# Kernel tuning notes

Hardware: AMD Instinct MI355X
Metric: run time of the kernel (lower is better)

The kernel has to match this reference:

```python
import jax, jax.numpy as jnp
import numpy as np

B, N, D_IN, D_B, K = 32, 1024, 1024, 256, 16384


def setup_inputs() -> dict:
    key = jax.random.key(0)
    ks = jax.random.split(key, 8)
    s_in = 1.0 / np.sqrt(D_IN)
    s_b = 1.0 / np.sqrt(D_B)
    return {
        "x": jax.random.normal(ks[0], (B, N, D_IN), dtype=jnp.float32),
        "W_in": jax.random.uniform(ks[1], (D_IN, D_B), jnp.float32, -s_in, s_in),
        "b_in": jax.random.uniform(ks[2], (D_B,), jnp.float32, -s_in, s_in),
        "W_out": jax.random.uniform(ks[3], (D_B, D_IN), jnp.float32, -s_b, s_b),
        "b_out": jax.random.uniform(ks[4], (D_IN,), jnp.float32, -s_b, s_b),
        "codebook": jax.random.normal(ks[5], (K, D_B), dtype=jnp.float32),
        "W_proj": jax.random.uniform(ks[6], (D_B, D_B), jnp.float32, -s_b, s_b),
        "b_proj": jax.random.uniform(ks[7], (D_B,), jnp.float32, -s_b, s_b),
    }


def reference(x, W_in, b_in, W_out, b_out, codebook, W_proj, b_proj):
    # project_in
    z = jnp.einsum('bnd,de->bne', x, W_in) + b_in            # [B,N,Db]
    # SimVQ: projected codebook
    emb = codebook @ W_proj + b_proj                          # [K,Db]
    zf = z.reshape(-1, z.shape[-1])                           # [B*N,Db]
    # squared-distance argmin (cdist pattern)
    d = (jnp.sum(zf**2, axis=1, keepdims=True)
         + jnp.sum(emb**2, axis=1)
         - 2.0 * zf @ emb.T)                                  # [B*N,K]
    q_idx = jnp.argmin(d, axis=1)                             # [B*N]
    quantized = emb[q_idx].reshape(z.shape)                   # [B,N,Db]
    # straight-through
    reg_z = z + jax.lax.stop_gradient(quantized - z)
    # project_out
    x_hat = jnp.einsum('bnd,de->bne', reg_z, W_out) + b_out   # [B,N,Dout]
    bottleneck_rep = q_idx.reshape(z.shape[0], z.shape[1])
    return x_hat, bottleneck_rep, z, emb, reg_z
```

## Files before the change

kernel.cpp:

```cpp
#include <hip/hip_runtime.h>

typedef unsigned int u32;
typedef unsigned long long u64;
typedef unsigned short u16;

#define M_ROWS 32768
#define DB 256
#define DIN 1024
#define KCODES 16384

typedef __attribute__((ext_vector_type(8))) short bf16x8;
typedef __attribute__((ext_vector_type(4))) float f32x4;
typedef __attribute__((ext_vector_type(8))) unsigned short us8;

#define GLOAD16(gp, lp) __builtin_amdgcn_global_load_lds( \
    (const __attribute__((address_space(1))) unsigned int*)(gp), \
    (__attribute__((address_space(3))) unsigned int*)(lp), 16, 0, 0)

__device__ __forceinline__ u32 ford(float f) {
    u32 u = __float_as_uint(f);
    return (u & 0x80000000u) ? ~u : (u | 0x80000000u);
}
__device__ __forceinline__ u64 shfl_xor_u64(u64 v, int m) {
    u32 lo = (u32)v, hi = (u32)(v >> 32);
    lo = (u32)__shfl_xor((int)lo, m, 64);
    hi = (u32)__shfl_xor((int)hi, m, 64);
    return ((u64)hi << 32) | lo;
}
__device__ __forceinline__ u16 f2bf_rne(float f) {
    const u32 u = __float_as_uint(f);
    return (u16)((u + 0x7FFFu + ((u >> 16) & 1u)) >> 16);
}

__global__ __launch_bounds__(256)
void sgemm_f32(const float* __restrict__ A, int lda,
               const float* __restrict__ B, int ldb,
               const float* __restrict__ bias,
               float* __restrict__ C, int ldc, int Kd)
{
    __shared__ float As[16][132];
    __shared__ float Bs[16][132];
    const int t = threadIdx.x;
    const int w = t >> 6, lane = t & 63;
    const int tx = (lane & 7) | ((w & 1) << 3);
    const int ty = ((lane >> 3) & 7) | ((w >> 1) << 3);
    const int rb = blockIdx.x << 7;
    const int cb = blockIdx.y << 7;

    const int sr  = t >> 1;
    const int sk8 = (t & 1) << 3;
    const int bkr = t >> 4;
    const int bc8 = (t & 15) << 3;

    const float* Ap = A + (size_t)(rb + sr) * lda + sk8;
    const float* Bp = B + (size_t)bkr * ldb + cb + bc8;

    float acc[8][8];
#pragma unroll
    for (int i = 0; i < 8; ++i)
#pragma unroll
        for (int j = 0; j < 8; ++j) acc[i][j] = 0.0f;

    float4 a0 = *(const float4*)Ap;
    float4 a1 = *(const float4*)(Ap + 4);
    float4 b0 = *(const float4*)Bp;
    float4 b1 = *(const float4*)(Bp + 4);

    for (int kb = 0; kb < Kd; kb += 16) {
        __syncthreads();
        As[sk8 + 0][sr] = a0.x; As[sk8 + 1][sr] = a0.y;
        As[sk8 + 2][sr] = a0.z; As[sk8 + 3][sr] = a0.w;
        As[sk8 + 4][sr] = a1.x; As[sk8 + 5][sr] = a1.y;
        As[sk8 + 6][sr] = a1.z; As[sk8 + 7][sr] = a1.w;
        *(float4*)&Bs[bkr][bc8]     = b0;
        *(float4*)&Bs[bkr][bc8 + 4] = b1;
        __syncthreads();
        if (kb + 16 < Kd) {
            a0 = *(const float4*)(Ap + kb + 16);
            a1 = *(const float4*)(Ap + kb + 20);
            b0 = *(const float4*)(Bp + (size_t)(kb + 16) * ldb);
            b1 = *(const float4*)(Bp + (size_t)(kb + 16) * ldb + 4);
        }
#pragma unroll
        for (int kk = 0; kk < 16; ++kk) {
            float a[8], b[8];
            *(float4*)&a[0] = *(const float4*)&As[kk][ty * 8];
            *(float4*)&a[4] = *(const float4*)&As[kk][ty * 8 + 4];
            *(float4*)&b[0] = *(const float4*)&Bs[kk][tx * 8];
            *(float4*)&b[4] = *(const float4*)&Bs[kk][tx * 8 + 4];
#pragma unroll
            for (int i = 0; i < 8; ++i)
#pragma unroll
                for (int j = 0; j < 8; ++j)
                    acc[i][j] += a[i] * b[j];
        }
    }

    float bb[8];
#pragma unroll
    for (int j = 0; j < 8; ++j) bb[j] = bias[cb + tx * 8 + j];

#pragma unroll
    for (int i = 0; i < 8; ++i) {
        const size_t off = (size_t)(rb + ty * 8 + i) * ldc + cb + tx * 8;
        *(float4*)&C[off]     = make_float4(acc[i][0] + bb[0], acc[i][1] + bb[1],
                                            acc[i][2] + bb[2], acc[i][3] + bb[3]);
        *(float4*)&C[off + 4] = make_float4(acc[i][4] + bb[4], acc[i][5] + bb[5],
                                            acc[i][6] + bb[6], acc[i][7] + bb[7]);
    }
}

__global__ __launch_bounds__(256)
void rowsq_kernel(const float* __restrict__ X, float* __restrict__ s2)
{
    const int t = threadIdx.x;
    const int row = (blockIdx.x << 2) + (t >> 6);
    const int lane = t & 63;
    const float4 v = *(const float4*)(X + (size_t)row * DB + (lane << 2));
    float s = v.x * v.x + v.y * v.y + v.z * v.z + v.w * v.w;
#pragma unroll
    for (int m = 32; m >= 1; m >>= 1) s += __shfl_xor(s, m, 64);
    if (lane == 0) s2[row] = s;
}

__global__ __launch_bounds__(256)
void split_pack(const float* __restrict__ X, u16* __restrict__ hi, u16* __restrict__ lo)
{
    const int tid = (blockIdx.x << 8) + threadIdx.x;
    const int row = tid >> 5;
    const int kb  = (tid & 31) << 3;
    const float4 v0 = *(const float4*)(X + ((size_t)row << 8) + kb);
    const float4 v1 = *(const float4*)(X + ((size_t)row << 8) + kb + 4);
    const float f[8] = {v0.x, v0.y, v0.z, v0.w, v1.x, v1.y, v1.z, v1.w};
    us8 hv, lv;
#pragma unroll
    for (int e = 0; e < 8; ++e) {
        const u16 h = f2bf_rne(f[e]);
        const float hf = __uint_as_float((u32)h << 16);
        hv[e] = h;
        lv[e] = f2bf_rne(f[e] - hf);
    }
    const size_t off = ((size_t)(row >> 4) * 8 + (kb >> 5)) * 512
                     + (size_t)((kb >> 3) & 3) * 128 + ((row & 15) << 3);
    *(us8*)(hi + off) = hv;
    *(us8*)(lo + off) = lv;
}

__global__ __launch_bounds__(256)
void score_mfma(const u16* __restrict__ zh, const u16* __restrict__ zl,
                const u16* __restrict__ eh, const u16* __restrict__ el,
                const float* __restrict__ e2, const float* __restrict__ z2,
                u64* __restrict__ partial)
{
    __shared__ u16 smem[4][8][512];
    const int t = threadIdx.x;
    const int w = t >> 6, lane = t & 63;
    const int wr = w >> 1, wc = w & 1;
    const int rb = blockIdx.x << 7, cb = blockIdx.y << 7;
    const u32 lane8 = (u32)lane << 3;

    const u32 zc0 = (u32)((rb >> 4) + w)     * 4096 + lane8;
    const u32 zc1 = (u32)((rb >> 4) + 4 + w) * 4096 + lane8;
    const u32 ec0 = (u32)((cb >> 4) + w)     * 4096 + lane8;
    const u32 ec1 = (u32)((cb >> 4) + 4 + w) * 4096 + lane8;

    u16* ZhL0 = &smem[0][w][0];      u16* ZhL1 = &smem[0][4 + w][0];
    u16* ZlL0 = &smem[1][w][0];      u16* ZlL1 = &smem[1][4 + w][0];
    u16* EhL0 = &smem[2][w][0];      u16* EhL1 = &smem[2][4 + w][0];
    u16* ElL0 = &smem[3][w][0];      u16* ElL1 = &smem[3][4 + w][0];

    f32x4 acc[4][4];
#pragma unroll
    for (int i = 0; i < 4; ++i)
#pragma unroll
        for (int j = 0; j < 4; ++j) acc[i][j] = (f32x4){0.f, 0.f, 0.f, 0.f};

    for (int ks = 0; ks < 8; ++ks) {
        const u32 ko = (u32)ks << 9;
        if (ks) __syncthreads();
        GLOAD16(zh + zc0 + ko, ZhL0);  GLOAD16(zh + zc1 + ko, ZhL1);
        GLOAD16(zl + zc0 + ko, ZlL0);  GLOAD16(zl + zc1 + ko, ZlL1);
        GLOAD16(eh + ec0 + ko, EhL0);  GLOAD16(eh + ec1 + ko, EhL1);
        GLOAD16(el + ec0 + ko, ElL0);  GLOAD16(el + ec1 + ko, ElL1);
        __syncthreads();

        bf16x8 ah[4], al[4], bh[4], bl[4];
#pragma unroll
        for (int i = 0; i < 4; ++i) {
            ah[i] = *(const bf16x8*)&smem[0][wr * 4 + i][lane8];
            al[i] = *(const bf16x8*)&smem[1][wr * 4 + i][lane8];
            bh[i] = *(const bf16x8*)&smem[2][wc * 4 + i][lane8];
            bl[i] = *(const bf16x8*)&smem[3][wc * 4 + i][lane8];
        }
#pragma unroll
        for (int i = 0; i < 4; ++i)
#pragma unroll
            for (int j = 0; j < 4; ++j) {
                acc[i][j] = __builtin_amdgcn_mfma_f32_16x16x32_bf16(ah[i], bh[j], acc[i][j], 0, 0, 0);
                acc[i][j] = __builtin_amdgcn_mfma_f32_16x16x32_bf16(ah[i], bl[j], acc[i][j], 0, 0, 0);
                acc[i][j] = __builtin_amdgcn_mfma_f32_16x16x32_bf16(al[i], bh[j], acc[i][j], 0, 0, 0);
            }
    }

    const int g = lane >> 4, li = lane & 15;
    float e2v[4];
#pragma unroll
    for (int j = 0; j < 4; ++j) e2v[j] = e2[cb + wc * 64 + j * 16 + li];
    const int slot = (blockIdx.y << 1) + wc;

#pragma unroll
    for (int i = 0; i < 4; ++i) {
#pragma unroll
        for (int r = 0; r < 4; ++r) {
            const int row = rb + wr * 64 + i * 16 + g * 4 + r;
            const float z2v = z2[row];
            u64 key = ~0ull;
#pragma unroll
            for (int j = 0; j < 4; ++j) {
                const float d = (z2v + e2v[j]) - 2.0f * acc[i][j][r];
                const u32 code = (u32)(cb + wc * 64 + j * 16 + li);
                const u64 k = ((u64)ford(d) << 32) | code;
                key = (k < key) ? k : key;
            }
#pragma unroll
            for (int m = 1; m <= 8; m <<= 1) {
                const u64 o = shfl_xor_u64(key, m);
                key = (o < key) ? o : key;
            }
            if (li == 0) partial[((size_t)row << 8) + slot] = key;
        }
    }
}

__global__ __launch_bounds__(256)
void finalize2(const u64* __restrict__ partial, const float* __restrict__ Z,
               const float* __restrict__ E, const float* __restrict__ z2,
               const float* __restrict__ e2,
               float* __restrict__ bneck, float* __restrict__ regz,
               int* __restrict__ qidx)
{
    const int t = threadIdx.x;
    const int row = (blockIdx.x << 2) + (t >> 6);
    const int lane = t & 63;
    const u64* p = partial + ((size_t)row << 8);

    u64 a1 = ~0ull, a2 = ~0ull;
#pragma unroll
    for (int q = 0; q < 4; ++q) {
        const u64 k = p[(q << 6) + lane];
        if (k < a1) { a2 = a1; a1 = k; }
        else if (k < a2) { a2 = k; }
    }
#pragma unroll
    for (int m = 1; m <= 32; m <<= 1) {
        const u64 b1 = shfl_xor_u64(a1, m);
        const u64 b2 = shfl_xor_u64(a2, m);
        if (b1 < a1) { a2 = (a1 < b2) ? a1 : b2; a1 = b1; }
        else         { a2 = (a2 < b1) ? a2 : b1; }
    }
    const u32 i1 = (u32)a1 & (KCODES - 1);
    const u32 i2 = (u32)a2 & (KCODES - 1);

    const float4 zv  = *(const float4*)(Z + ((size_t)row << 8) + (lane << 2));
    const float4 c1v = *(const float4*)(E + ((size_t)i1 << 8) + (lane << 2));
    const float4 c2v = *(const float4*)(E + ((size_t)i2 << 8) + (lane << 2));
    float s1 = zv.x * c1v.x + zv.y * c1v.y + zv.z * c1v.z + zv.w * c1v.w;
    float s2 = zv.x * c2v.x + zv.y * c2v.y + zv.z * c2v.z + zv.w * c2v.w;
#pragma unroll
    for (int m = 32; m >= 1; m >>= 1) {
        s1 += __shfl_xor(s1, m, 64);
        s2 += __shfl_xor(s2, m, 64);
    }
    const float zz = z2[row];
    const float d1 = (zz + e2[i1]) - 2.0f * s1;
    const float d2 = (zz + e2[i2]) - 2.0f * s2;
    u32 win = i1;
    if (d2 < d1 || (d2 == d1 && i2 < i1)) win = i2;

    if (lane == 0) { qidx[row] = (int)win; bneck[row] = (float)win; }
    const float4 vw = *(const float4*)(E + ((size_t)win << 8) + (lane << 2));
    *(float4*)(regz + ((size_t)row << 8) + (lane << 2)) = vw;
}

__global__ __launch_bounds__(256)
void xhat_gemm(const int* __restrict__ qidx, const float* __restrict__ E,
               const float* __restrict__ B, const float* __restrict__ bias,
               float* __restrict__ C)
{
    __shared__ float As[16][132];
    __shared__ float Bs[16][132];
    const int t = threadIdx.x;
    const int w = t >> 6, lane = t & 63;
    const int tx = (lane & 7) | ((w & 1) << 3);
    const int ty = ((lane >> 3) & 7) | ((w >> 1) << 3);
    const int rb = blockIdx.x << 7;
    const int cb = blockIdx.y << 7;

    const int sr  = t >> 1;
    const int sk8 = (t & 1) << 3;
    const int bkr = t >> 4;
    const int bc8 = (t & 15) << 3;

    const int aidx = qidx[rb + sr] & (KCODES - 1);
    const float* Ap = E + (size_t)aidx * DB + sk8;
    const float* Bp = B + (size_t)bkr * DIN + cb + bc8;

    float acc[8][8];
#pragma unroll
    for (int i = 0; i < 8; ++i)
#pragma unroll
        for (int j = 0; j < 8; ++j) acc[i][j] = 0.0f;

    float4 a0 = *(const float4*)Ap;
    float4 a1 = *(const float4*)(Ap + 4);
    float4 b0 = *(const float4*)Bp;
    float4 b1 = *(const float4*)(Bp + 4);

    for (int kb = 0; kb < DB; kb += 16) {
        __syncthreads();
        As[sk8 + 0][sr] = a0.x; As[sk8 + 1][sr] = a0.y;
        As[sk8 + 2][sr] = a0.z; As[sk8 + 3][sr] = a0.w;
        As[sk8 + 4][sr] = a1.x; As[sk8 + 5][sr] = a1.y;
        As[sk8 + 6][sr] = a1.z; As[sk8 + 7][sr] = a1.w;
        *(float4*)&Bs[bkr][bc8]     = b0;
        *(float4*)&Bs[bkr][bc8 + 4] = b1;
        __syncthreads();
        if (kb + 16 < DB) {
            a0 = *(const float4*)(Ap + kb + 16);
            a1 = *(const float4*)(Ap + kb + 20);
            b0 = *(const float4*)(Bp + (size_t)(kb + 16) * DIN);
            b1 = *(const float4*)(Bp + (size_t)(kb + 16) * DIN + 4);
        }
#pragma unroll
        for (int kk = 0; kk < 16; ++kk) {
            float a[8], b[8];
            *(float4*)&a[0] = *(const float4*)&As[kk][ty * 8];
            *(float4*)&a[4] = *(const float4*)&As[kk][ty * 8 + 4];
            *(float4*)&b[0] = *(const float4*)&Bs[kk][tx * 8];
            *(float4*)&b[4] = *(const float4*)&Bs[kk][tx * 8 + 4];
#pragma unroll
            for (int i = 0; i < 8; ++i)
#pragma unroll
                for (int j = 0; j < 8; ++j)
                    acc[i][j] += a[i] * b[j];
        }
    }

    float bb[8];
#pragma unroll
    for (int j = 0; j < 8; ++j) bb[j] = bias[cb + tx * 8 + j];

#pragma unroll
    for (int i = 0; i < 8; ++i) {
        const size_t off = (size_t)(rb + ty * 8 + i) * DIN + cb + tx * 8;
        *(float4*)&C[off]     = make_float4(acc[i][0] + bb[0], acc[i][1] + bb[1],
                                            acc[i][2] + bb[2], acc[i][3] + bb[3]);
        *(float4*)&C[off + 4] = make_float4(acc[i][4] + bb[4], acc[i][5] + bb[5],
                                            acc[i][6] + bb[6], acc[i][7] + bb[7]);
    }
}

extern "C" void kernel_launch(void* const* d_in, const int* in_sizes, int n_in,
                              void* d_out, int out_size, void* d_ws, size_t ws_size,
                              hipStream_t stream)
{
    const float* x        = (const float*)d_in[0];
    const float* W_in     = (const float*)d_in[1];
    const float* b_in     = (const float*)d_in[2];
    const float* W_out    = (const float*)d_in[3];
    const float* b_out    = (const float*)d_in[4];
    const float* codebook = (const float*)d_in[5];
    const float* W_proj   = (const float*)d_in[6];
    const float* b_proj   = (const float*)d_in[7];

    float* out   = (float*)d_out;
    float* xhat  = out;
    float* bneck = out + 33554432;
    float* z     = out + 33587200;
    float* emb   = out + 41975808;
    float* regz  = out + 46170112;

    char* outc = (char*)d_out;
    u64* partial = (u64*)outc;
    u16* eh = (u16*)(outc + 67108864);
    u16* el = (u16*)(outc + 75497472);
    u16* zh = (u16*)(outc + 184680448);
    u16* zl = (u16*)(outc + 201457664);

    char* ws = (char*)d_ws;
    float* e2   = (float*)ws;
    float* z2   = (float*)(ws + 65536);
    int*   qidx = (int*)  (ws + 196608);

    sgemm_f32<<<dim3(128, 2), 256, 0, stream>>>(codebook, DB, W_proj, DB, b_proj,
                                                emb, DB, DB);
    rowsq_kernel<<<KCODES / 4, 256, 0, stream>>>(emb, e2);
    sgemm_f32<<<dim3(256, 2), 256, 0, stream>>>(x, DIN, W_in, DB, b_in,
                                                z, DB, DIN);
    rowsq_kernel<<<M_ROWS / 4, 256, 0, stream>>>(z, z2);
    split_pack<<<M_ROWS / 8, 256, 0, stream>>>(z, zh, zl);
    split_pack<<<KCODES / 8, 256, 0, stream>>>(emb, eh, el);
    score_mfma<<<dim3(M_ROWS / 128, KCODES / 128), 256, 0, stream>>>(
        zh, zl, eh, el, e2, z2, partial);
    finalize2<<<M_ROWS / 4, 256, 0, stream>>>(partial, z, emb, z2, e2,
                                              bneck, regz, qidx);
    xhat_gemm<<<dim3(256, 8), 256, 0, stream>>>(qidx, emb, W_out, b_out, xhat);
}
```

Before: 1.633 ms.

## Precompute projected codebook through W_out and gather x_hat rows; fuse row norms

Since quantized rows are codebook rows, x_hat is computed by multiplying the whole projected codebook by W_out once with split-bf16 MFMA and then gathering rows by index. This replaces the large fp32 SIMT output GEMM over all tokens. Row squared norms are fused into the split/pack kernels, and the score epilogue folds -e2/2 into the accumulator init and takes a max, dropping z2. The fast path needs a large workspace buffer and falls back to the old GEMM otherwise.

```diff
diff --git a/kernel.cpp b/kernel.cpp
--- a/kernel.cpp
+++ b/kernel.cpp
@@ -111,20 +111,8 @@
 }
 
 __global__ __launch_bounds__(256)
-void rowsq_kernel(const float* __restrict__ X, float* __restrict__ s2)
-{
-    const int t = threadIdx.x;
-    const int row = (blockIdx.x << 2) + (t >> 6);
-    const int lane = t & 63;
-    const float4 v = *(const float4*)(X + (size_t)row * DB + (lane << 2));
-    float s = v.x * v.x + v.y * v.y + v.z * v.z + v.w * v.w;
-#pragma unroll
-    for (int m = 32; m >= 1; m >>= 1) s += __shfl_xor(s, m, 64);
-    if (lane == 0) s2[row] = s;
-}
-
-__global__ __launch_bounds__(256)
-void split_pack(const float* __restrict__ X, u16* __restrict__ hi, u16* __restrict__ lo)
+void split_pack(const float* __restrict__ X, u16* __restrict__ hi,
+                u16* __restrict__ lo, float* __restrict__ s2)
 {
     const int tid = (blockIdx.x << 8) + threadIdx.x;
     const int row = tid >> 5;
@@ -133,24 +121,48 @@
     const float4 v1 = *(const float4*)(X + ((size_t)row << 8) + kb + 4);
     const float f[8] = {v0.x, v0.y, v0.z, v0.w, v1.x, v1.y, v1.z, v1.w};
     us8 hv, lv;
+    float s = 0.0f;
 #pragma unroll
     for (int e = 0; e < 8; ++e) {
         const u16 h = f2bf_rne(f[e]);
         const float hf = __uint_as_float((u32)h << 16);
         hv[e] = h;
         lv[e] = f2bf_rne(f[e] - hf);
+        s += f[e] * f[e];
     }
     const size_t off = ((size_t)(row >> 4) * 8 + (kb >> 5)) * 512
                      + (size_t)((kb >> 3) & 3) * 128 + ((row & 15) << 3);
     *(us8*)(hi + off) = hv;
     *(us8*)(lo + off) = lv;
+#pragma unroll
+    for (int m = 1; m <= 16; m <<= 1) s += __shfl_xor(s, m, 64);
+    if ((threadIdx.x & 31) == 0) s2[row] = s;
+}
+
+__global__ __launch_bounds__(256)
+void pack_wout(const float* __restrict__ W, u16* __restrict__ hi, u16* __restrict__ lo)
+{
+    const int tid = (blockIdx.x << 8) + threadIdx.x;
+    const int n  = tid >> 5;
+    const int kb = (tid & 31) << 3;
+    us8 hv, lv;
+#pragma unroll
+    for (int e = 0; e < 8; ++e) {
+        const float f = W[(size_t)(kb + e) * DIN + n];
+        const u16 h = f2bf_rne(f);
+        hv[e] = h;
+        lv[e] = f2bf_rne(f - __uint_as_float((u32)h << 16));
+    }
+    const size_t off = ((size_t)(n >> 4) * 8 + (kb >> 5)) * 512
+                     + (size_t)((kb >> 3) & 3) * 128 + ((n & 15) << 3);
+    *(us8*)(hi + off) = hv;
+    *(us8*)(lo + off) = lv;
 }
 
 __global__ __launch_bounds__(256)
 void score_mfma(const u16* __restrict__ zh, const u16* __restrict__ zl,
                 const u16* __restrict__ eh, const u16* __restrict__ el,
-                const float* __restrict__ e2, const float* __restrict__ z2,
-                u64* __restrict__ partial)
+                const float* __restrict__ e2, u64* __restrict__ partial)
 {
     __shared__ u16 smem[4][8][512];
     const int t = threadIdx.x;
@@ -158,6 +170,7 @@
     const int wr = w >> 1, wc = w & 1;
     const int rb = blockIdx.x << 7, cb = blockIdx.y << 7;
     const u32 lane8 = (u32)lane << 3;
+    const int g = lane >> 4, li = lane & 15;
 
     const u32 zc0 = (u32)((rb >> 4) + w)     * 4096 + lane8;
     const u32 zc1 = (u32)((rb >> 4) + 4 + w) * 4096 + lane8;
@@ -169,11 +182,22 @@
     u16* EhL0 = &smem[2][w][0];      u16* EhL1 = &smem[2][4 + w][0];
     u16* ElL0 = &smem[3][w][0];      u16* ElL1 = &smem[3][4 + w][0];
 
+    int codes[4];
+    float e2v[4];
+#pragma unroll
+    for (int j = 0; j < 4; ++j) {
+        codes[j] = cb + wc * 64 + j * 16 + li;
+        e2v[j] = e2[codes[j]];
+    }
+
     f32x4 acc[4][4];
 #pragma unroll
     for (int i = 0; i < 4; ++i)
 #pragma unroll
-        for (int j = 0; j < 4; ++j) acc[i][j] = (f32x4){0.f, 0.f, 0.f, 0.f};
+        for (int j = 0; j < 4; ++j) {
+            const float v = -0.5f * e2v[j];
+            acc[i][j] = (f32x4){v, v, v, v};
+        }
 
     for (int ks = 0; ks < 8; ++ks) {
         const u32 ko = (u32)ks << 9;
@@ -202,10 +226,6 @@
             }
     }
 
-    const int g = lane >> 4, li = lane & 15;
-    float e2v[4];
-#pragma unroll
-    for (int j = 0; j < 4; ++j) e2v[j] = e2[cb + wc * 64 + j * 16 + li];
     const int slot = (blockIdx.y << 1) + wc;
 
 #pragma unroll
@@ -213,15 +233,13 @@
 #pragma unroll
         for (int r = 0; r < 4; ++r) {
             const int row = rb + wr * 64 + i * 16 + g * 4 + r;
-            const float z2v = z2[row];
-            u64 key = ~0ull;
-#pragma unroll
-            for (int j = 0; j < 4; ++j) {
-                const float d = (z2v + e2v[j]) - 2.0f * acc[i][j][r];
-                const u32 code = (u32)(cb + wc * 64 + j * 16 + li);
-                const u64 k = ((u64)ford(d) << 32) | code;
-                key = (k < key) ? k : key;
-            }
+            const float s0 = acc[i][0][r], s1 = acc[i][1][r];
+            const float s2s = acc[i][2][r], s3 = acc[i][3][r];
+            const float mm = fmaxf(fmaxf(s0, s1), fmaxf(s2s, s3));
+            const u32 cj = (mm == s0) ? (u32)codes[0]
+                         : (mm == s1) ? (u32)codes[1]
+                         : (mm == s2s) ? (u32)codes[2] : (u32)codes[3];
+            u64 key = ((u64)ford(-mm) << 32) | cj;
 #pragma unroll
             for (int m = 1; m <= 8; m <<= 1) {
                 const u64 o = shfl_xor_u64(key, m);
@@ -280,6 +298,89 @@
     if (lane == 0) { qidx[row] = (int)win; bneck[row] = (float)win; }
     const float4 vw = *(const float4*)(E + ((size_t)win << 8) + (lane << 2));
     *(float4*)(regz + ((size_t)row << 8) + (lane << 2)) = vw;
+}
+
+__global__ __launch_bounds__(256)
+void embout_mfma(const u16* __restrict__ ah_p, const u16* __restrict__ al_p,
+                 const u16* __restrict__ bh_p, const u16* __restrict__ bl_p,
+                 const float* __restrict__ bias, float* __restrict__ C)
+{
+    __shared__ u16 smem[4][8][512];
+    const int t = threadIdx.x;
+    const int w = t >> 6, lane = t & 63;
+    const int wr = w >> 1, wc = w & 1;
+    const int rb = blockIdx.x << 7, cb = blockIdx.y << 7;
+    const u32 lane8 = (u32)lane << 3;
+    const int g = lane >> 4, li = lane & 15;
+
+    const u32 ac0 = (u32)((rb >> 4) + w)     * 4096 + lane8;
+    const u32 ac1 = (u32)((rb >> 4) + 4 + w) * 4096 + lane8;
+    const u32 bc0 = (u32)((cb >> 4) + w)     * 4096 + lane8;
+    const u32 bc1 = (u32)((cb >> 4) + 4 + w) * 4096 + lane8;
+
+    u16* AhL0 = &smem[0][w][0];      u16* AhL1 = &smem[0][4 + w][0];
+    u16* AlL0 = &smem[1][w][0];      u16* AlL1 = &smem[1][4 + w][0];
+    u16* BhL0 = &smem[2][w][0];      u16* BhL1 = &smem[2][4 + w][0];
+    u16* BlL0 = &smem[3][w][0];      u16* BlL1 = &smem[3][4 + w][0];
+
+    f32x4 acc[4][4];
+#pragma unroll
+    for (int i = 0; i < 4; ++i)
+#pragma unroll
+        for (int j = 0; j < 4; ++j) acc[i][j] = (f32x4){0.f, 0.f, 0.f, 0.f};
+
+    for (int ks = 0; ks < 8; ++ks) {
+        const u32 ko = (u32)ks << 9;
+        if (ks) __syncthreads();
+        GLOAD16(ah_p + ac0 + ko, AhL0);  GLOAD16(ah_p + ac1 + ko, AhL1);
+        GLOAD16(al_p + ac0 + ko, AlL0);  GLOAD16(al_p + ac1 + ko, AlL1);
+        GLOAD16(bh_p + bc0 + ko, BhL0);  GLOAD16(bh_p + bc1 + ko, BhL1);
+        GLOAD16(bl_p + bc0 + ko, BlL0);  GLOAD16(bl_p + bc1 + ko, BlL1);
+        __syncthreads();
+
+        bf16x8 ah[4], al[4], bh[4], bl[4];
+#pragma unroll
+        for (int i = 0; i < 4; ++i) {
+            ah[i] = *(const bf16x8*)&smem[0][wr * 4 + i][lane8];
+            al[i] = *(const bf16x8*)&smem[1][wr * 4 + i][lane8];
+            bh[i] = *(const bf16x8*)&smem[2][wc * 4 + i][lane8];
+            bl[i] = *(const bf16x8*)&smem[3][wc * 4 + i][lane8];
+        }
+#pragma unroll
+        for (int i = 0; i < 4; ++i)
+#pragma unroll
+            for (int j = 0; j < 4; ++j) {
+                acc[i][j] = __builtin_amdgcn_mfma_f32_16x16x32_bf16(ah[i], bh[j], acc[i][j], 0, 0, 0);
+                acc[i][j] = __builtin_amdgcn_mfma_f32_16x16x32_bf16(ah[i], bl[j], acc[i][j], 0, 0, 0);
+                acc[i][j] = __builtin_amdgcn_mfma_f32_16x16x32_bf16(al[i], bh[j], acc[i][j], 0, 0, 0);
+            }
+    }
+
+    float bv[4];
+#pragma unroll
+    for (int j = 0; j < 4; ++j) bv[j] = bias[cb + wc * 64 + j * 16 + li];
+
+#pragma unroll
+    for (int i = 0; i < 4; ++i)
+#pragma unroll
+        for (int j = 0; j < 4; ++j) {
+            const int col = cb + wc * 64 + j * 16 + li;
+#pragma unroll
+            for (int r = 0; r < 4; ++r) {
+                const int m = rb + wr * 64 + i * 16 + g * 4 + r;
+                C[(size_t)m * DIN + col] = acc[i][j][r] + bv[j];
+            }
+        }
+}
+
+__global__ __launch_bounds__(256)
+void gather_rows(const int* __restrict__ qidx, const float* __restrict__ S,
+                 float* __restrict__ D)
+{
+    const int row = blockIdx.x;
+    const int q = qidx[row] & (KCODES - 1);
+    const float4 v = *(const float4*)(S + ((size_t)q << 10) + (threadIdx.x << 2));
+    *(float4*)(D + ((size_t)row << 10) + (threadIdx.x << 2)) = v;
 }
 
 __global__ __launch_bounds__(256)
@@ -391,18 +492,29 @@
     float* e2   = (float*)ws;
     float* z2   = (float*)(ws + 65536);
     int*   qidx = (int*)  (ws + 196608);
+    u16*   whh     = (u16*)  (ws + 327680);
+    u16*   whl     = (u16*)  (ws + 851968);
+    float* emb_out = (float*)(ws + 1376256);
+    const bool fast_xhat = (ws_size >= (size_t)1376256 + 67108864);
 
     sgemm_f32<<<dim3(128, 2), 256, 0, stream>>>(codebook, DB, W_proj, DB, b_proj,
                                                 emb, DB, DB);
-    rowsq_kernel<<<KCODES / 4, 256, 0, stream>>>(emb, e2);
+    split_pack<<<KCODES / 8, 256, 0, stream>>>(emb, eh, el, e2);
+    if (fast_xhat) {
+        pack_wout<<<DIN / 8, 256, 0, stream>>>(W_out, whh, whl);
+        embout_mfma<<<dim3(KCODES / 128, DIN / 128), 256, 0, stream>>>(
+            eh, el, whh, whl, b_out, emb_out);
+    }
     sgemm_f32<<<dim3(256, 2), 256, 0, stream>>>(x, DIN, W_in, DB, b_in,
                                                 z, DB, DIN);
-    rowsq_kernel<<<M_ROWS / 4, 256, 0, stream>>>(z, z2);
-    split_pack<<<M_ROWS / 8, 256, 0, stream>>>(z, zh, zl);
-    split_pack<<<KCODES / 8, 256, 0, stream>>>(emb, eh, el);
+    split_pack<<<M_ROWS / 8, 256, 0, stream>>>(z, zh, zl, z2);
     score_mfma<<<dim3(M_ROWS / 128, KCODES / 128), 256, 0, stream>>>(
-        zh, zl, eh, el, e2, z2, partial);
+        zh, zl, eh, el, e2, partial);
     finalize2<<<M_ROWS / 4, 256, 0, stream>>>(partial, z, emb, z2, e2,
                                               bneck, regz, qidx);
-    xhat_gemm<<<dim3(256, 8), 256, 0, stream>>>(qidx, emb, W_out, b_out, xhat);
-}
+    if (fast_xhat) {
+        gather_rows<<<M_ROWS, 256, 0, stream>>>(qidx, emb_out, xhat);
+    } else {
+        xhat_gemm<<<dim3(256, 8), 256, 0, stream>>>(qidx, emb, W_out, b_out, xhat);
+    }
+}
```

Measured after the change: 1.411 ms. 13.6% less time.
